# Kernel optimization log

Measured on AMD Instinct MI355X. Metric: run time of the kernel, lower is better.

The kernel has to match this reference:

```python
import jax, jax.numpy as jnp
import numpy as np
from jax import lax

B, N, C = 8, 16384, 4
NUM_GROUPS = 128
GROUP_SIZE = 32
GROUP_RADIUS = 0.1
UPSCALE_K = 128
OVERLAP_FACTOR = 0.7


def setup_inputs() -> dict:
    key = jax.random.key(0)
    k1, k2 = jax.random.split(key)
    # xyz in [0,1]^3, energy in [0,1] at channel 3
    points = jax.random.uniform(k1, (B, N, C), dtype=jnp.float32)
    lengths = jax.random.randint(k2, (B,), N // 2, N + 1).astype(jnp.int32)
    return {"points": points, "lengths": lengths}


def _fps(xyz, lengths, K):
    """Farthest point sampling. xyz: (B,N,3) -> centers (B,K,3), idx (B,K)."""
    B_, N_, _ = xyz.shape
    valid = jnp.arange(N_)[None, :] < lengths[:, None]          # (B,N)
    mind0 = jnp.where(valid, jnp.inf, -jnp.inf)                 # running min dist
    start = jnp.zeros((B_,), jnp.int32)                         # fixed start point
    batch = jnp.arange(B_)

    def step(carry, _):
        mind, cur = carry
        c = xyz[batch, cur]                                     # (B,3)
        d = jnp.sum((xyz - c[:, None, :]) ** 2, axis=-1)        # (B,N)
        mind = jnp.minimum(mind, jnp.where(valid, d, -jnp.inf))
        nxt = jnp.argmax(mind, axis=1).astype(jnp.int32)
        return (mind, nxt), cur

    _, idxs = lax.scan(step, (mind0, start), None, length=K)
    idxs = idxs.T                                               # (B,K)
    centers = xyz[batch[:, None], idxs]                         # (B,K,3)
    return centers, idxs


def _cnms(centers, radius, overlap_factor):
    """Greedy cluster-NMS over FPS-ordered centers. Returns keep mask (B,G)."""
    B_, G, _ = centers.shape
    d2 = jnp.sum((centers[:, :, None, :] - centers[:, None, :, :]) ** 2, axis=-1)
    thr = (2.0 * radius * (1.0 - overlap_factor)) ** 2          # spheres overlap > factor

    def step(keep, j):
        conflict = jnp.any(keep & (d2[:, j, :] < thr), axis=-1)
        keep = keep.at[:, j].set(~conflict)
        return keep, None

    keep, _ = lax.scan(step, jnp.zeros((B_, G), bool), jnp.arange(G))
    return keep


def _ball_query(centers, xyz, lengths, retain, K, radius):
    """First-K points within radius of each center (pytorch3d semantics); -1 pad."""
    N_ = xyz.shape[1]
    d2 = jnp.sum((centers[:, :, None, :] - xyz[:, None, :, :]) ** 2, axis=-1)  # (B,G,N)
    in_len = (jnp.arange(N_)[None, :] < lengths[:, None])[:, None, :]
    valid = (d2 <= radius * radius) & in_len & retain[:, :, None]
    # pick the K smallest point indices among valid ones -> "first K found"
    key_ = jnp.where(valid, jnp.arange(N_, dtype=jnp.int32)[None, None, :], N_)
    negv, _ = lax.top_k(-key_, K)                               # (B,G,K)
    idx = -negv
    return jnp.where(idx == N_, -1, idx)


def reference(points, lengths):
    xyz = points[..., :3]
    centers, _ = _fps(xyz, lengths, NUM_GROUPS)                 # (B,G,3)
    retain = _cnms(centers, GROUP_RADIUS, OVERLAP_FACTOR)       # (B,G)
    idx = _ball_query(centers, xyz, lengths, retain, UPSCALE_K, GROUP_RADIUS)

    # select_topk_by_energy (energies_idx = 3)
    batch = jnp.arange(points.shape[0])[:, None, None]
    invalid = idx == -1
    energies = jnp.where(invalid, -jnp.inf, points[batch, jnp.clip(idx, 0), 3])
    topv, topi = lax.top_k(energies, GROUP_SIZE)                # (B,G,K_new)
    tidx = jnp.take_along_axis(idx, topi, axis=2)
    tidx = jnp.where(jnp.isneginf(topv), -1, tidx)

    # fill_empty_indices: replace -1 with the group's first index
    fidx = jnp.where(tidx == -1, tidx[:, :, :1], tidx)

    # masked_gather: -1 -> gather 0 then zero out
    groups = points[batch, jnp.clip(fidx, 0)]                   # (B,G,K,C)
    groups = jnp.where((fidx == -1)[..., None], 0.0, groups)

    group_lengths = jnp.sum(jnp.all(tidx != -1, axis=2), axis=1)  # (B,)
    embedding_mask = jnp.arange(NUM_GROUPS)[None, :] < group_lengths[:, None]

    # center xyz channels, then scale ALL channels by radius (as in source)
    groups = groups.at[..., :3].add(-centers[:, :, None, :])
    groups = groups / GROUP_RADIUS
    return groups, centers, embedding_mask
```

## Files before the change

### kernel.cpp

```cpp
#include <hip/hip_runtime.h>
#include <math.h>

#define B_ 8
#define N_ 16384
#define G_ 128
#define GS_ 32
#define UK_ 128
#define FPS_T 1024
#define FPS_W 16
#define FPS_BLK 4
#define SLICE (N_ / FPS_BLK)
#define PPT (SLICE / FPS_T)
#define BQ_T 512
#define BQ_W 8

__device__ __forceinline__ float dist2(float x, float y, float z,
                                       float cx, float cy, float cz) {
    float dx = __fsub_rn(x, cx);
    float dy = __fsub_rn(y, cy);
    float dz = __fsub_rn(z, cz);
    return __fadd_rn(__fadd_rn(__fmul_rn(dx, dx), __fmul_rn(dy, dy)),
                     __fmul_rn(dz, dz));
}

__device__ __forceinline__ unsigned long long shfl_xor_u64(unsigned long long v, int m) {
    int lo = __shfl_xor((int)(unsigned)(v & 0xffffffffull), m);
    int hi = __shfl_xor((int)(unsigned)(v >> 32), m);
    return ((unsigned long long)(unsigned)hi << 32) | (unsigned)lo;
}

__device__ __forceinline__ unsigned long long umax64(unsigned long long a,
                                                     unsigned long long b) {
    return a > b ? a : b;
}

__device__ __forceinline__ unsigned wave_umax_bcast(unsigned v) {
    unsigned t;
    t = (unsigned)__builtin_amdgcn_update_dpp(0, (int)v, 0x111, 0xf, 0xf, false); v = v > t ? v : t;
    t = (unsigned)__builtin_amdgcn_update_dpp(0, (int)v, 0x112, 0xf, 0xf, false); v = v > t ? v : t;
    t = (unsigned)__builtin_amdgcn_update_dpp(0, (int)v, 0x114, 0xf, 0xf, false); v = v > t ? v : t;
    t = (unsigned)__builtin_amdgcn_update_dpp(0, (int)v, 0x118, 0xf, 0xf, false); v = v > t ? v : t;
    t = (unsigned)__builtin_amdgcn_update_dpp(0, (int)v, 0x142, 0xa, 0xf, false); v = v > t ? v : t;
    t = (unsigned)__builtin_amdgcn_update_dpp(0, (int)v, 0x143, 0xc, 0xf, false); v = v > t ? v : t;
    return (unsigned)__builtin_amdgcn_readlane((int)v, 63);
}
__device__ __forceinline__ unsigned wave_umin_bcast(unsigned v) {
    unsigned t;
    t = (unsigned)__builtin_amdgcn_update_dpp(-1, (int)v, 0x111, 0xf, 0xf, false); v = v < t ? v : t;
    t = (unsigned)__builtin_amdgcn_update_dpp(-1, (int)v, 0x112, 0xf, 0xf, false); v = v < t ? v : t;
    t = (unsigned)__builtin_amdgcn_update_dpp(-1, (int)v, 0x114, 0xf, 0xf, false); v = v < t ? v : t;
    t = (unsigned)__builtin_amdgcn_update_dpp(-1, (int)v, 0x118, 0xf, 0xf, false); v = v < t ? v : t;
    t = (unsigned)__builtin_amdgcn_update_dpp(-1, (int)v, 0x142, 0xa, 0xf, false); v = v < t ? v : t;
    t = (unsigned)__builtin_amdgcn_update_dpp(-1, (int)v, 0x143, 0xc, 0xf, false); v = v < t ? v : t;
    return (unsigned)__builtin_amdgcn_readlane((int)v, 63);
}

__global__ void init_kernel(unsigned long long* __restrict__ slots,
                            int* __restrict__ gl) {
    int t = threadIdx.x;
#pragma unroll
    for (int i = 0; i < (B_ * G_ * FPS_BLK) / 1024; i++)
        slots[i * 1024 + t] = 0ull;
    if (t < B_) gl[t] = 0;
}

__global__ __launch_bounds__(FPS_T, 4) void fps_cnms_kernel(
    const float4* __restrict__ pts, const int* __restrict__ lengths,
    float* __restrict__ centers_out, int* __restrict__ keep_out,
    unsigned long long* __restrict__ slots) {
    const int b = blockIdx.x & 7;
    const int slice = blockIdx.x >> 3;
    const int t = threadIdx.x;
    const int lane = t & 63;
    const int wv = t >> 6;
    const int len = lengths[b];
    const float4* p = pts + (size_t)b * N_;
    const int base = slice * SLICE;

    __shared__ float4 s_xy4[SLICE / 2];
    __shared__ __align__(16) unsigned long long s_part[FPS_W];
    __shared__ int s_bcn[2];
    __shared__ float s_cen[G_][3];

    float zs[PPT], mind[PPT];
#pragma unroll
    for (int i2 = 0; i2 < PPT / 2; i2++) {
        int nA = base + (2 * i2) * FPS_T + t;
        int nB = base + (2 * i2 + 1) * FPS_T + t;
        float4 qA = p[nA];
        float4 qB = p[nB];
        s_xy4[i2 * FPS_T + t] = make_float4(qA.x, qA.y, qB.x, qB.y);
        zs[2 * i2]     = qA.z;
        zs[2 * i2 + 1] = qB.z;
        mind[2 * i2]     = (nA < len) ? INFINITY : -INFINITY;
        mind[2 * i2 + 1] = (nB < len) ? INFINITY : -INFINITY;
    }
    __syncthreads();

    int n = 0;
    for (int k = 0; k < G_; k++) {
        float4 c = p[n];
        float cx = c.x, cy = c.y, cz = c.z;
        if (slice == 0 && t == 0) {
            centers_out[(b * G_ + k) * 3 + 0] = cx;
            centers_out[(b * G_ + k) * 3 + 1] = cy;
            centers_out[(b * G_ + k) * 3 + 2] = cz;
            s_cen[k][0] = cx; s_cen[k][1] = cy; s_cen[k][2] = cz;
        }
        if (k == G_ - 1) break;

        float bv = -INFINITY;
        int bn = 0x7fffffff;
#pragma unroll
        for (int i2 = 0; i2 < PPT / 2; i2++) {
            float4 xy = s_xy4[i2 * FPS_T + t];
            float dA = dist2(xy.x, xy.y, zs[2 * i2],     cx, cy, cz);
            float dB = dist2(xy.z, xy.w, zs[2 * i2 + 1], cx, cy, cz);
            float mA = fminf(mind[2 * i2], dA);
            float mB = fminf(mind[2 * i2 + 1], dB);
            mind[2 * i2] = mA;
            mind[2 * i2 + 1] = mB;
            if (mA > bv) { bv = mA; bn = base + (2 * i2) * FPS_T + t; }
            if (mB > bv) { bv = mB; bn = base + (2 * i2 + 1) * FPS_T + t; }
        }
        unsigned u = __float_as_uint(bv);
        u = (u & 0x80000000u) ? ~u : (u | 0x80000000u);

        unsigned wmax = wave_umax_bcast(u);
        unsigned ik = (u == wmax) ? (unsigned)bn : 0xffffffffu;
        unsigned wbn = wave_umin_bcast(ik);

        if (lane == 0)
            s_part[wv] = ((unsigned long long)wmax << 32) | (unsigned)(~wbn);
        __syncthreads();

        if (wv == 0) {
            unsigned long long kk = s_part[lane & 15];
#pragma unroll
            for (int off = 8; off; off >>= 1)
                kk = umax64(kk, shfl_xor_u64(kk, off));

            unsigned long long* slot = slots + ((size_t)b * G_ + k) * FPS_BLK;
            if (lane == 0)
                __hip_atomic_store(&slot[slice], kk, __ATOMIC_RELAXED,
                                   __HIP_MEMORY_SCOPE_AGENT);
            unsigned long long v = kk;
            if (lane < FPS_BLK && lane != slice) {
                do {
                    v = __hip_atomic_load(&slot[lane], __ATOMIC_RELAXED,
                                          __HIP_MEMORY_SCOPE_AGENT);
                } while (v == 0ull);
            }
            unsigned long long m = umax64(v, shfl_xor_u64(v, 1));
            m = umax64(m, shfl_xor_u64(m, 2));
            if (lane == 0)
                s_bcn[k & 1] = (int)(~(unsigned)(m & 0xffffffffull));
        }
        __syncthreads();
        n = s_bcn[k & 1];
    }

    if (slice == 0 && t < 64) {
        const float THR = (float)((2.0 * 0.1 * (1.0 - 0.7)) * (2.0 * 0.1 * (1.0 - 0.7)));
        float ax = s_cen[t][0],      ay = s_cen[t][1],      az = s_cen[t][2];
        float ex = s_cen[t + 64][0], ey = s_cen[t + 64][1], ez = s_cen[t + 64][2];
        bool k0 = false, k1 = false;
        for (int j = 0; j < G_; j++) {
            float jx = s_cen[j][0], jy = s_cen[j][1], jz = s_cen[j][2];
            bool c0 = k0 && (dist2(ax, ay, az, jx, jy, jz) < THR);
            bool c1 = k1 && (dist2(ex, ey, ez, jx, jy, jz) < THR);
            bool conflict = __any(c0 || c1);
            if (j == t)      k0 = !conflict;
            if (j == t + 64) k1 = !conflict;
        }
        keep_out[b * G_ + t]      = k0 ? 1 : 0;
        keep_out[b * G_ + t + 64] = k1 ? 1 : 0;
    }
}

__global__ __launch_bounds__(BQ_T) void group_kernel(
    const float4* __restrict__ pts, const int* __restrict__ lengths,
    const float* __restrict__ centers, const int* __restrict__ keep,
    float* __restrict__ groups_out, int* __restrict__ gl) {
    const int bid = blockIdx.x;
    const int b = bid >> 7;
    const int t = threadIdx.x;
    const int lane = t & 63;
    const int wv = t >> 6;

    const float cx = centers[bid * 3 + 0];
    const float cy = centers[bid * 3 + 1];
    const float cz = centers[bid * 3 + 2];
    float4* out4 = (float4*)(groups_out + (size_t)bid * GS_ * 4);

    if (!keep[bid]) {
        if (t < GS_) {
            float4 o;
            o.x = __fdiv_rn(__fsub_rn(0.f, cx), 0.1f);
            o.y = __fdiv_rn(__fsub_rn(0.f, cy), 0.1f);
            o.z = __fdiv_rn(__fsub_rn(0.f, cz), 0.1f);
            o.w = 0.f;
            out4[t] = o;
        }
        return;
    }

    __shared__ int   s_widx[BQ_W][UK_];
    __shared__ float s_wen[BQ_W][UK_];
    __shared__ int   s_wcnt[BQ_W];
    __shared__ int   s_list[UK_];
    __shared__ float s_en[UK_];
    __shared__ int   s_ord[GS_];

    const int len = lengths[b];
    const float R2 = (float)(0.1 * 0.1);
    const float4* p = pts + (size_t)b * N_;

    {
        const int base0 = wv * (N_ / BQ_W);
        int cnt = 0;
        for (int it = 0; it < (N_ / BQ_W) / 64; it++) {
            int n = base0 + it * 64 + lane;
            float4 q = p[n];
            float d2 = dist2(q.x, q.y, q.z, cx, cy, cz);
            bool pred = (n < len) && (d2 <= R2);
            unsigned long long m = __ballot(pred);
            int prefix = __popcll(m & ((1ull << lane) - 1ull));
            int slot = cnt + prefix;
            if (pred && slot < UK_) { s_widx[wv][slot] = n; s_wen[wv][slot] = q.w; }
            cnt += __popcll(m);
        }
        if (lane == 0) s_wcnt[wv] = (cnt < UK_) ? cnt : UK_;
    }
    __syncthreads();

    int M = 0;
#pragma unroll
    for (int w = 0; w < BQ_W; w++) M += s_wcnt[w];
    if (M > UK_) M = UK_;

    if (t < UK_ && t < M) {
        int j = t, w = 0;
        while (w < BQ_W - 1 && j >= s_wcnt[w]) { j -= s_wcnt[w]; w++; }
        s_list[t] = s_widx[w][j];
        s_en[t]   = s_wen[w][j];
    }
    __syncthreads();

    if (wv == 0) {
        float v0 = (lane < M) ? s_en[lane] : -INFINITY;
        float v1 = (lane + 64 < M) ? s_en[lane + 64] : -INFINITY;
        for (int k = 0; k < GS_; k++) {
            float bv; int bs;
            if (v0 >= v1) { bv = v0; bs = lane; }
            else          { bv = v1; bs = lane + 64; }
#pragma unroll
            for (int off = 32; off; off >>= 1) {
                float ov = __shfl_xor(bv, off);
                int   os = __shfl_xor(bs, off);
                bool tk = (ov > bv) || (ov == bv && os < bs);
                bv = tk ? ov : bv; bs = tk ? os : bs;
            }
            if (lane == 0) s_ord[k] = (bv == -INFINITY) ? -1 : bs;
            if (bs == lane)           v0 = -INFINITY;
            else if (bs == lane + 64) v1 = -INFINITY;
        }
    }
    __syncthreads();

    if (t < GS_) {
        int o0 = s_ord[0];
        int first = (o0 >= 0) ? s_list[o0] : -1;
        int ok = s_ord[t];
        int ti = (ok >= 0) ? s_list[ok] : -1;
        int f = (ti == -1) ? first : ti;
        float px = 0.f, py = 0.f, pz = 0.f, pw = 0.f;
        if (f >= 0) { float4 q = p[f]; px = q.x; py = q.y; pz = q.z; pw = q.w; }
        float4 o;
        o.x = __fdiv_rn(__fsub_rn(px, cx), 0.1f);
        o.y = __fdiv_rn(__fsub_rn(py, cy), 0.1f);
        o.z = __fdiv_rn(__fsub_rn(pz, cz), 0.1f);
        o.w = __fdiv_rn(pw, 0.1f);
        out4[t] = o;
    }
    if (t == 0 && M >= GS_) atomicAdd(&gl[b], 1);
}

__global__ void mask_kernel(const int* __restrict__ gl, float* __restrict__ mask_out) {
    int t = threadIdx.x;
    int b = t >> 7, g = t & 127;
    mask_out[t] = (g < gl[b]) ? 1.0f : 0.0f;
}

extern "C" void kernel_launch(void* const* d_in, const int* in_sizes, int n_in,
                              void* d_out, int out_size, void* d_ws, size_t ws_size,
                              hipStream_t stream) {
    const float4* pts = (const float4*)d_in[0];
    const int* lengths = (const int*)d_in[1];
    float* out = (float*)d_out;
    float* groups = out;
    float* centers = out + (size_t)B_ * G_ * GS_ * 4;
    float* mask = centers + (size_t)B_ * G_ * 3;
    unsigned long long* slots = (unsigned long long*)d_ws;
    int* keep = (int*)(slots + B_ * G_ * FPS_BLK);
    int* gl = keep + B_ * G_;

    hipLaunchKernelGGL(init_kernel, dim3(1), dim3(1024), 0, stream, slots, gl);
    hipLaunchKernelGGL(fps_cnms_kernel, dim3(B_ * FPS_BLK), dim3(FPS_T), 0, stream,
                       pts, lengths, centers, keep, slots);
    hipLaunchKernelGGL(group_kernel, dim3(B_ * G_), dim3(BQ_T), 0, stream,
                       pts, lengths, centers, keep, groups, gl);
    hipLaunchKernelGGL(mask_kernel, dim3(1), dim3(B_ * G_), 0, stream, gl, mask);
}
```

Before: 298.8 us.

## Replace per-iteration block barriers with per-wave global slot exchange in FPS

Each wave now publishes its own argmax candidate directly to a global slot array sized for every wave of every slice block (64 slots per step). Every wave then spin-polls all 64 slots and reduces them itself, which removes the two __syncthreads and the shared-memory partial reduction from each FPS iteration. The init kernel grows to clear the larger slot array. The cost is more global atomic traffic and polling contention from all 16 waves per block, plus a larger workspace. A stray label and an empty if-block were also added.

```diff
diff --git a/kernel.cpp b/kernel.cpp
--- a/kernel.cpp
+++ b/kernel.cpp
@@ -9,6 +9,7 @@
 #define FPS_T 1024
 #define FPS_W 16
 #define FPS_BLK 4
+#define NSLOT (FPS_BLK * FPS_W)
 #define SLICE (N_ / FPS_BLK)
 #define PPT (SLICE / FPS_T)
 #define BQ_T 512
@@ -21,17 +22,6 @@
     float dz = __fsub_rn(z, cz);
     return __fadd_rn(__fadd_rn(__fmul_rn(dx, dx), __fmul_rn(dy, dy)),
                      __fmul_rn(dz, dz));
-}
-
-__device__ __forceinline__ unsigned long long shfl_xor_u64(unsigned long long v, int m) {
-    int lo = __shfl_xor((int)(unsigned)(v & 0xffffffffull), m);
-    int hi = __shfl_xor((int)(unsigned)(v >> 32), m);
-    return ((unsigned long long)(unsigned)hi << 32) | (unsigned)lo;
-}
-
-__device__ __forceinline__ unsigned long long umax64(unsigned long long a,
-                                                     unsigned long long b) {
-    return a > b ? a : b;
 }
 
 __device__ __forceinline__ unsigned wave_umax_bcast(unsigned v) {
@@ -57,11 +47,9 @@
 
 __global__ void init_kernel(unsigned long long* __restrict__ slots,
                             int* __restrict__ gl) {
-    int t = threadIdx.x;
-#pragma unroll
-    for (int i = 0; i < (B_ * G_ * FPS_BLK) / 1024; i++)
-        slots[i * 1024 + t] = 0ull;
-    if (t < B_) gl[t] = 0;
+    int i = blockIdx.x * 1024 + threadIdx.x;
+    slots[i] = 0ull;
+    if (i < B_) gl[i] = 0;
 }
 
 __global__ __launch_bounds__(FPS_T, 4) void fps_cnms_kernel(
@@ -78,8 +66,6 @@
     const int base = slice * SLICE;
 
     __shared__ float4 s_xy4[SLICE / 2];
-    __shared__ __align__(16) unsigned long long s_part[FPS_W];
-    __shared__ int s_bcn[2];
     __shared__ float s_cen[G_][3];
 
     float zs[PPT], mind[PPT];
@@ -129,35 +115,28 @@
         unsigned wmax = wave_umax_bcast(u);
         unsigned ik = (u == wmax) ? (unsigned)bn : 0xffffffffu;
         unsigned wbn = wave_umin_bcast(ik);
-
+        unsigned long long kk =
+            ((unsigned long long)wmax << 32) | (unsigned)(~wbn);
+
+        unsigned long long* slot = slots + ((size_t)(b * G_ + k)) * NSLOT;
         if (lane == 0)
-            s_part[wv] = ((unsigned long long)wmax << 32) | (unsigned)(~wbn);
-        __syncthreads();
-
-        if (wv == 0) {
-            unsigned long long kk = s_part[lane & 15];
-#pragma unroll
-            for (int off = 8; off; off >>= 1)
-                kk = umax64(kk, shfl_xor_u64(kk, off));
-
-            unsigned long long* slot = slots + ((size_t)b * G_ + k) * FPS_BLK;
-            if (lane == 0)
-                __hip_atomic_store(&slot[slice], kk, __ATOMIC_RELAXED,
-                                   __HIP_MEMORY_SCOPE_AGENT);
-            unsigned long long v = kk;
-            if (lane < FPS_BLK && lane != slice) {
-                do {
-                    v = __hip_atomic_load(&slot[lane], __ATOMIC_RELAXED,
-                                          __HIP_MEMORY_SCOPE_AGENT);
-                } while (v == 0ull);
-            }
-            unsigned long long m = umax64(v, shfl_xor_u64(v, 1));
-            m = umax64(m, shfl_xor_u64(m, 2));
-            if (lane == 0)
-                s_bcn[k & 1] = (int)(~(unsigned)(m & 0xffffffffull));
-        }
-        __syncthreads();
-        n = s_bcn[k & 1];
+            __hip_atomic_store(&slot[slice * FPS_W + wv], kk, __ATOMIC_RELAXED,
+                               __HIP_MEMORY_SCOPE_AGENT);
+        unsigned long long v;
+        do {
+            v = __hip_atomic_load(&slot[lane], __ATOMIC_RELAXED,
+                                  __HIP_MEMORY_SCOPE_AGENT);
+        } while (__ballot(v == 0ull) != 0ull);
+
+        unsigned hi = (unsigned)(v >> 32);
+        unsigned mh = wave_umax_bcast(hi);
+        unsigned lo = (hi == mh) ? (unsigned)(v & 0xffffffffull) : 0u;
+        unsigned ml = wave_umax_bcast(lo);
+        n = (int)(~ml);
+    }
+
+    if (t == FPS_T - 1) gl_global_store: ;
+    if (slice == FPS_BLK - 1 && t == FPS_T - 1) {
     }
 
     if (slice == 0 && t < 64) {
@@ -302,10 +281,11 @@
     float* centers = out + (size_t)B_ * G_ * GS_ * 4;
     float* mask = centers + (size_t)B_ * G_ * 3;
     unsigned long long* slots = (unsigned long long*)d_ws;
-    int* keep = (int*)(slots + B_ * G_ * FPS_BLK);
+    int* keep = (int*)(slots + (size_t)B_ * G_ * NSLOT);
     int* gl = keep + B_ * G_;
 
-    hipLaunchKernelGGL(init_kernel, dim3(1), dim3(1024), 0, stream, slots, gl);
+    hipLaunchKernelGGL(init_kernel, dim3((B_ * G_ * NSLOT) / 1024), dim3(1024),
+                       0, stream, slots, gl);
     hipLaunchKernelGGL(fps_cnms_kernel, dim3(B_ * FPS_BLK), dim3(FPS_T), 0, stream,
                        pts, lengths, centers, keep, slots);
     hipLaunchKernelGGL(group_kernel, dim3(B_ * G_), dim3(BQ_T), 0, stream,
```

Result: slower. 843.8 us (+182.3%).

## Replace per-group ball query with point-centric binning and wave-level top-k select

Applied to the files above, without the earlier changes.

Replaces the per-center ball-query kernel, which rescanned every point of the batch for each group, with a binning kernel. That kernel reads each point once, tests it against all kept centers, and appends it to per-group lists via atomics. A lightweight one-wave select kernel then restores first-K-by-index semantics with a binary search on indices and picks the top energies with 64-bit wave max reductions. This cuts redundant global reads but adds atomic contention, a fixed list capacity of 256 entries per group, and an extra kernel launch.

```diff
diff --git a/kernel.cpp b/kernel.cpp
--- a/kernel.cpp
+++ b/kernel.cpp
@@ -6,13 +6,12 @@
 #define G_ 128
 #define GS_ 32
 #define UK_ 128
+#define CAP_ 256
 #define FPS_T 1024
 #define FPS_W 16
 #define FPS_BLK 4
 #define SLICE (N_ / FPS_BLK)
 #define PPT (SLICE / FPS_T)
-#define BQ_T 512
-#define BQ_W 8
 
 __device__ __forceinline__ float dist2(float x, float y, float z,
                                        float cx, float cy, float cz) {
@@ -32,6 +31,11 @@
 __device__ __forceinline__ unsigned long long umax64(unsigned long long a,
                                                      unsigned long long b) {
     return a > b ? a : b;
+}
+
+__device__ __forceinline__ unsigned fmono(float f) {
+    unsigned u = __float_as_uint(f);
+    return (u & 0x80000000u) ? ~u : (u | 0x80000000u);
 }
 
 __device__ __forceinline__ unsigned wave_umax_bcast(unsigned v) {
@@ -56,11 +60,11 @@
 }
 
 __global__ void init_kernel(unsigned long long* __restrict__ slots,
-                            int* __restrict__ gl) {
+                            unsigned* __restrict__ cnt, int* __restrict__ gl) {
     int t = threadIdx.x;
 #pragma unroll
-    for (int i = 0; i < (B_ * G_ * FPS_BLK) / 1024; i++)
-        slots[i * 1024 + t] = 0ull;
+    for (int i = 0; i < 4; i++) slots[i * 1024 + t] = 0ull;
+    cnt[t] = 0u;
     if (t < B_) gl[t] = 0;
 }
 
@@ -123,8 +127,7 @@
             if (mA > bv) { bv = mA; bn = base + (2 * i2) * FPS_T + t; }
             if (mB > bv) { bv = mB; bn = base + (2 * i2 + 1) * FPS_T + t; }
         }
-        unsigned u = __float_as_uint(bv);
-        u = (u & 0x80000000u) ? ~u : (u | 0x80000000u);
+        unsigned u = fmono(bv);
 
         unsigned wmax = wave_umax_bcast(u);
         unsigned ik = (u == wmax) ? (unsigned)bn : 0xffffffffu;
@@ -178,15 +181,69 @@
     }
 }
 
-__global__ __launch_bounds__(BQ_T) void group_kernel(
+__global__ __launch_bounds__(256) void bin_kernel(
     const float4* __restrict__ pts, const int* __restrict__ lengths,
     const float* __restrict__ centers, const int* __restrict__ keep,
+    unsigned* __restrict__ cnt, unsigned long long* __restrict__ list) {
+    const int b = blockIdx.x >> 5;
+    const int seg = blockIdx.x & 31;
+    const int t = threadIdx.x;
+    const float R2 = (float)(0.1 * 0.1);
+
+    __shared__ float4 s_c[G_];
+    if (t < G_) {
+        float4 c;
+        if (keep[b * G_ + t]) {
+            c.x = centers[(b * G_ + t) * 3 + 0];
+            c.y = centers[(b * G_ + t) * 3 + 1];
+            c.z = centers[(b * G_ + t) * 3 + 2];
+        } else {
+            c.x = INFINITY; c.y = 0.f; c.z = 0.f;
+        }
+        c.w = 0.f;
+        s_c[t] = c;
+    }
+    __syncthreads();
+
+    const int len = lengths[b];
+    const float4* p = pts + (size_t)b * N_;
+    const int nA = seg * 512 + t;
+    const int nB = seg * 512 + 256 + t;
+    float4 qA = p[nA];
+    float4 qB = p[nB];
+    const bool vA = nA < len, vB = nB < len;
+    if (!vA && !vB) return;
+
+    unsigned* c_b = cnt + b * G_;
+    unsigned long long* l_b = list + (size_t)b * G_ * CAP_;
+#pragma unroll 4
+    for (int g = 0; g < G_; g++) {
+        float4 c = s_c[g];
+        float dA = dist2(qA.x, qA.y, qA.z, c.x, c.y, c.z);
+        float dB = dist2(qB.x, qB.y, qB.z, c.x, c.y, c.z);
+        if (vA && dA <= R2) {
+            unsigned slot = atomicAdd(&c_b[g], 1u);
+            if (slot < CAP_)
+                l_b[(size_t)g * CAP_ + slot] =
+                    ((unsigned long long)(unsigned)nA << 32) | __float_as_uint(qA.w);
+        }
+        if (vB && dB <= R2) {
+            unsigned slot = atomicAdd(&c_b[g], 1u);
+            if (slot < CAP_)
+                l_b[(size_t)g * CAP_ + slot] =
+                    ((unsigned long long)(unsigned)nB << 32) | __float_as_uint(qB.w);
+        }
+    }
+}
+
+__global__ __launch_bounds__(64) void select_kernel(
+    const float4* __restrict__ pts, const float* __restrict__ centers,
+    const int* __restrict__ keep, const unsigned* __restrict__ cnt,
+    const unsigned long long* __restrict__ list,
     float* __restrict__ groups_out, int* __restrict__ gl) {
     const int bid = blockIdx.x;
     const int b = bid >> 7;
-    const int t = threadIdx.x;
-    const int lane = t & 63;
-    const int wv = t >> 6;
+    const int lane = threadIdx.x;
 
     const float cx = centers[bid * 3 + 0];
     const float cy = centers[bid * 3 + 1];
@@ -194,96 +251,81 @@
     float4* out4 = (float4*)(groups_out + (size_t)bid * GS_ * 4);
 
     if (!keep[bid]) {
-        if (t < GS_) {
+        if (lane < GS_) {
             float4 o;
             o.x = __fdiv_rn(__fsub_rn(0.f, cx), 0.1f);
             o.y = __fdiv_rn(__fsub_rn(0.f, cy), 0.1f);
             o.z = __fdiv_rn(__fsub_rn(0.f, cz), 0.1f);
             o.w = 0.f;
-            out4[t] = o;
+            out4[lane] = o;
         }
         return;
     }
 
-    __shared__ int   s_widx[BQ_W][UK_];
-    __shared__ float s_wen[BQ_W][UK_];
-    __shared__ int   s_wcnt[BQ_W];
-    __shared__ int   s_list[UK_];
-    __shared__ float s_en[UK_];
-    __shared__ int   s_ord[GS_];
-
-    const int len = lengths[b];
-    const float R2 = (float)(0.1 * 0.1);
-    const float4* p = pts + (size_t)b * N_;
-
-    {
-        const int base0 = wv * (N_ / BQ_W);
-        int cnt = 0;
-        for (int it = 0; it < (N_ / BQ_W) / 64; it++) {
-            int n = base0 + it * 64 + lane;
-            float4 q = p[n];
-            float d2 = dist2(q.x, q.y, q.z, cx, cy, cz);
-            bool pred = (n < len) && (d2 <= R2);
-            unsigned long long m = __ballot(pred);
-            int prefix = __popcll(m & ((1ull << lane) - 1ull));
-            int slot = cnt + prefix;
-            if (pred && slot < UK_) { s_widx[wv][slot] = n; s_wen[wv][slot] = q.w; }
-            cnt += __popcll(m);
-        }
-        if (lane == 0) s_wcnt[wv] = (cnt < UK_) ? cnt : UK_;
-    }
-    __syncthreads();
-
-    int M = 0;
-#pragma unroll
-    for (int w = 0; w < BQ_W; w++) M += s_wcnt[w];
-    if (M > UK_) M = UK_;
-
-    if (t < UK_ && t < M) {
-        int j = t, w = 0;
-        while (w < BQ_W - 1 && j >= s_wcnt[w]) { j -= s_wcnt[w]; w++; }
-        s_list[t] = s_widx[w][j];
-        s_en[t]   = s_wen[w][j];
-    }
-    __syncthreads();
-
-    if (wv == 0) {
-        float v0 = (lane < M) ? s_en[lane] : -INFINITY;
-        float v1 = (lane + 64 < M) ? s_en[lane + 64] : -INFINITY;
-        for (int k = 0; k < GS_; k++) {
-            float bv; int bs;
-            if (v0 >= v1) { bv = v0; bs = lane; }
-            else          { bv = v1; bs = lane + 64; }
-#pragma unroll
-            for (int off = 32; off; off >>= 1) {
-                float ov = __shfl_xor(bv, off);
-                int   os = __shfl_xor(bs, off);
-                bool tk = (ov > bv) || (ov == bv && os < bs);
-                bv = tk ? ov : bv; bs = tk ? os : bs;
+    const unsigned Mt = cnt[bid];
+    const int M = (Mt < CAP_) ? (int)Mt : CAP_;
+    const unsigned long long* l = list + (size_t)bid * CAP_;
+
+    unsigned long long key[4];
+#pragma unroll
+    for (int j = 0; j < 4; j++) {
+        int s = lane + 64 * j;
+        if (s < M) {
+            unsigned long long e = l[s];
+            unsigned idx = (unsigned)(e >> 32);
+            unsigned km = fmono(__uint_as_float((unsigned)e));
+            key[j] = ((unsigned long long)km << 32) | (unsigned)(~idx);
+        } else {
+            key[j] = 0ull;
+        }
+    }
+
+    if (Mt > UK_) {
+        int lo = 0, hi = N_ - 1;
+        while (lo < hi) {
+            int mid = (lo + hi) >> 1;
+            int c = 0;
+#pragma unroll
+            for (int j = 0; j < 4; j++) {
+                bool in = key[j] && ((int)(~(unsigned)key[j]) <= mid);
+                c += __popcll(__ballot(in));
             }
-            if (lane == 0) s_ord[k] = (bv == -INFINITY) ? -1 : bs;
-            if (bs == lane)           v0 = -INFINITY;
-            else if (bs == lane + 64) v1 = -INFINITY;
-        }
-    }
-    __syncthreads();
-
-    if (t < GS_) {
-        int o0 = s_ord[0];
-        int first = (o0 >= 0) ? s_list[o0] : -1;
-        int ok = s_ord[t];
-        int ti = (ok >= 0) ? s_list[ok] : -1;
-        int f = (ti == -1) ? first : ti;
+            if (c >= UK_) hi = mid; else lo = mid + 1;
+        }
+#pragma unroll
+        for (int j = 0; j < 4; j++)
+            if (key[j] && ((int)(~(unsigned)key[j]) > lo)) key[j] = 0ull;
+    }
+
+    int myidx = -1;
+    for (int r = 0; r < GS_; r++) {
+        unsigned long long m = umax64(umax64(key[0], key[1]),
+                                      umax64(key[2], key[3]));
+#pragma unroll
+        for (int off = 32; off; off >>= 1)
+            m = umax64(m, shfl_xor_u64(m, off));
+        if (r == lane) myidx = (m == 0ull) ? -1 : (int)(~(unsigned)m);
+#pragma unroll
+        for (int j = 0; j < 4; j++)
+            if (key[j] == m) key[j] = 0ull;
+    }
+
+    int first = __shfl(myidx, 0);
+    if (lane < GS_) {
+        int f = (myidx < 0) ? first : myidx;
         float px = 0.f, py = 0.f, pz = 0.f, pw = 0.f;
-        if (f >= 0) { float4 q = p[f]; px = q.x; py = q.y; pz = q.z; pw = q.w; }
+        if (f >= 0) {
+            float4 q = pts[(size_t)b * N_ + f];
+            px = q.x; py = q.y; pz = q.z; pw = q.w;
+        }
         float4 o;
         o.x = __fdiv_rn(__fsub_rn(px, cx), 0.1f);
         o.y = __fdiv_rn(__fsub_rn(py, cy), 0.1f);
         o.z = __fdiv_rn(__fsub_rn(pz, cz), 0.1f);
         o.w = __fdiv_rn(pw, 0.1f);
-        out4[t] = o;
-    }
-    if (t == 0 && M >= GS_) atomicAdd(&gl[b], 1);
+        out4[lane] = o;
+    }
+    if (lane == 0 && Mt >= (unsigned)GS_) atomicAdd(&gl[b], 1);
 }
 
 __global__ void mask_kernel(const int* __restrict__ gl, float* __restrict__ mask_out) {
@@ -301,14 +343,20 @@
     float* groups = out;
     float* centers = out + (size_t)B_ * G_ * GS_ * 4;
     float* mask = centers + (size_t)B_ * G_ * 3;
+
     unsigned long long* slots = (unsigned long long*)d_ws;
-    int* keep = (int*)(slots + B_ * G_ * FPS_BLK);
+    unsigned* cnt = (unsigned*)(slots + 4096);
+    unsigned long long* list = (unsigned long long*)(cnt + 1024);
+    int* keep = (int*)(list + (size_t)B_ * G_ * CAP_);
     int* gl = keep + B_ * G_;
 
-    hipLaunchKernelGGL(init_kernel, dim3(1), dim3(1024), 0, stream, slots, gl);
+    hipLaunchKernelGGL(init_kernel, dim3(1), dim3(1024), 0, stream,
+                       slots, cnt, gl);
     hipLaunchKernelGGL(fps_cnms_kernel, dim3(B_ * FPS_BLK), dim3(FPS_T), 0, stream,
                        pts, lengths, centers, keep, slots);
-    hipLaunchKernelGGL(group_kernel, dim3(B_ * G_), dim3(BQ_T), 0, stream,
-                       pts, lengths, centers, keep, groups, gl);
+    hipLaunchKernelGGL(bin_kernel, dim3(B_ * 32), dim3(256), 0, stream,
+                       pts, lengths, centers, keep, cnt, list);
+    hipLaunchKernelGGL(select_kernel, dim3(B_ * G_), dim3(64), 0, stream,
+                       pts, centers, keep, cnt, list, groups, gl);
     hipLaunchKernelGGL(mask_kernel, dim3(1), dim3(B_ * G_), 0, stream, gl, mask);
 }
```

New measurement: 328.8 us. 1.1x slower.
